# Performance work log

Hardware: AMD Instinct MI355X
Metric: run time of the kernel (lower is better)

Reference implementation:

```python
import jax, jax.numpy as jnp
import numpy as np

CACHE_LEN = 1024
EPS = 1e-5

def layer_norm(x, g, b):
    m = jnp.mean(x, axis=-1, keepdims=True)
    var = jnp.mean(jnp.square(x - m), axis=-1, keepdims=True)
    return (x - m) * jax.lax.rsqrt(var + EPS) * g + b

def setup_inputs() -> dict:
    key = jax.random.key(0)
    ks = jax.random.split(key, 16)
    B, Lq, Lk, D_IN, D_OUT = 4, 4096, 5119, 512, 512
    s = 1.0 / np.sqrt(D_IN)
    return {
        "q": jax.random.normal(ks[0], (B, Lq, D_IN), jnp.float32),
        "k": jax.random.normal(ks[1], (B, Lk, D_IN), jnp.float32),
        "v": jax.random.normal(ks[2], (B, Lk, D_IN), jnp.float32),
        "gq": jnp.ones((D_IN,), jnp.float32),
        "bq": jnp.zeros((D_IN,), jnp.float32),
        "gk": jnp.ones((D_IN,), jnp.float32),
        "bk": jnp.zeros((D_IN,), jnp.float32),
        "gv": jnp.ones((D_IN,), jnp.float32),
        "bv": jnp.zeros((D_IN,), jnp.float32),
        "Wq": jax.random.uniform(ks[3], (D_IN, D_OUT), jnp.float32, -s, s),
        "bwq": jax.random.uniform(ks[4], (D_OUT,), jnp.float32, -s, s),
        "Wk": jax.random.uniform(ks[5], (D_IN, D_OUT), jnp.float32, -s, s),
        "bwk": jax.random.uniform(ks[6], (D_OUT,), jnp.float32, -s, s),
        "Wv": jax.random.uniform(ks[7], (D_IN, D_OUT), jnp.float32, -s, s),
        "bwv": jax.random.uniform(ks[8], (D_OUT,), jnp.float32, -s, s),
    }

def reference(q, k, v, gq, bq, gk, bk, gv, bv, Wq, bwq, Wk, bwk, Wv, bwv):
    B, Lq, _ = q.shape
    Lk = k.shape[1]
    qp = layer_norm(q, gq, bq) @ Wq + bwq            # [B,Lq,Do]
    kp = layer_norm(k, gk, bk) @ Wk + bwk            # [B,Lk,Do]
    vp = layer_norm(v, gv, bv) @ Wv + bwv            # [B,Lk,Do]
    kv = jax.nn.relu(kp) * vp                         # [B,Lk,Do]
    # integrate3 skew-pad builds a banded ones mask: query row i attends to
    # kv columns [sup+i, sup+i+cache_len-1]. Equivalent sliding-window sum
    # computed via prefix sums (O(Lk*d) instead of O(Lq*Lk*d)).
    sup = Lk - Lq - CACHE_LEN + 1
    cs = jnp.cumsum(kv, axis=1)
    cs = jnp.concatenate([jnp.zeros_like(cs[:, :1]), cs], axis=1)  # [B,Lk+1,Do]
    starts = sup + jnp.arange(Lq)
    weighted = cs[:, starts + CACHE_LEN] - cs[:, starts]            # [B,Lq,Do]
    return jax.nn.relu(qp) * weighted
```

## Files before the change

### kernel.cpp

```cpp
#include <hip/hip_runtime.h>

#define B     4
#define LQ    4096
#define LK    5119
#define LKP   5120
#define D     512
#define CACHE 1024
#define MQ    (B * LQ)
#define MKP   (B * LKP)
#define NCH   160
#define TI    32

typedef float  f32x4  __attribute__((ext_vector_type(4)));
typedef __bf16 bf16x2 __attribute__((ext_vector_type(2)));
typedef __bf16 bf16x4 __attribute__((ext_vector_type(4)));
typedef __bf16 bf16x8 __attribute__((ext_vector_type(8)));

__device__ __forceinline__ void async16(void* lds, const void* g)
{
    __builtin_amdgcn_global_load_lds(
        (__attribute__((address_space(1))) void*)(g),
        (__attribute__((address_space(3))) void*)(lds),
        16, 0, 0);
}

__global__ __launch_bounds__(256) void prep_kernel(
    const float* __restrict__ q, const float* __restrict__ k,
    const float* __restrict__ v,
    const float* __restrict__ gq, const float* __restrict__ bq,
    const float* __restrict__ gk, const float* __restrict__ bk,
    const float* __restrict__ gv, const float* __restrict__ bv,
    const float* __restrict__ Wq, const float* __restrict__ Wk,
    const float* __restrict__ Wv,
    __bf16* __restrict__ qn, __bf16* __restrict__ kn, __bf16* __restrict__ vn,
    __bf16* __restrict__ wtq, __bf16* __restrict__ wtk, __bf16* __restrict__ wtv)
{
    const int z = blockIdx.y;

    if (z == 3) {
        const int idx = blockIdx.x;
        if (idx >= 384) return;
        const int zz  = idx >> 7;
        const int rem = idx & 127;
        const float* W = (zz == 0) ? Wq : (zz == 1) ? Wk : Wv;
        __bf16*     Wt = (zz == 0) ? wtq : (zz == 1) ? wtk : wtv;
        const int n  = (rem & 1) * 256 + threadIdx.x;
        const int k0 = (rem >> 1) * 8;
        bf16x8 o;
#pragma unroll
        for (int j = 0; j < 8; ++j)
            o[j] = (__bf16)W[(long)(k0 + j) * D + n];
        *reinterpret_cast<bf16x8*>(Wt + (long)n * D + k0) = o;
        return;
    }

    const float *x, *g, *bb; __bf16* o;
    if (z == 0)      { x = q; g = gq; bb = bq; o = qn; }
    else if (z == 1) { x = k; g = gk; bb = bk; o = kn; }
    else             { x = v; g = gv; bb = bv; o = vn; }

    const int nrows = (z == 0) ? MQ : MKP;
    const int wid   = threadIdx.x >> 6;
    const int lane  = threadIdx.x & 63;
    const int rp    = blockIdx.x * 4 + wid;
    if (rp >= nrows) return;

    long rin; bool valid = true;
    if (z == 0) rin = rp;
    else {
        const int bch = rp / LKP;
        int i = rp - bch * LKP;
        if (i == LK) { valid = false; i = LK - 1; }
        rin = (long)bch * LK + i;
    }

    const int    c0 = lane * 4;
    const float* xr = x + rin * D;

    const float4 a0 = *reinterpret_cast<const float4*>(xr + c0);
    const float4 a1 = *reinterpret_cast<const float4*>(xr + 256 + c0);

    float s  = a0.x + a0.y + a0.z + a0.w + a1.x + a1.y + a1.z + a1.w;
    float ss = a0.x*a0.x + a0.y*a0.y + a0.z*a0.z + a0.w*a0.w
             + a1.x*a1.x + a1.y*a1.y + a1.z*a1.z + a1.w*a1.w;
#pragma unroll
    for (int m = 1; m <= 32; m <<= 1) {
        s  += __shfl_xor(s,  m, 64);
        ss += __shfl_xor(ss, m, 64);
    }
    const float mean = s * (1.f / (float)D);
    const float var  = ss * (1.f / (float)D) - mean * mean;
    const float rs   = rsqrtf(var + 1e-5f);

    const float4 g0 = *reinterpret_cast<const float4*>(g  + c0);
    const float4 g1 = *reinterpret_cast<const float4*>(g  + 256 + c0);
    const float4 b0 = *reinterpret_cast<const float4*>(bb + c0);
    const float4 b1 = *reinterpret_cast<const float4*>(bb + 256 + c0);

    bf16x4 o0, o1;
    o0[0] = (__bf16)((a0.x - mean) * rs * g0.x + b0.x);
    o0[1] = (__bf16)((a0.y - mean) * rs * g0.y + b0.y);
    o0[2] = (__bf16)((a0.z - mean) * rs * g0.z + b0.z);
    o0[3] = (__bf16)((a0.w - mean) * rs * g0.w + b0.w);
    o1[0] = (__bf16)((a1.x - mean) * rs * g1.x + b1.x);
    o1[1] = (__bf16)((a1.y - mean) * rs * g1.y + b1.y);
    o1[2] = (__bf16)((a1.z - mean) * rs * g1.z + b1.z);
    o1[3] = (__bf16)((a1.w - mean) * rs * g1.w + b1.w);

    if (valid) {
        __bf16* orow = o + (long)rp * D;
        *reinterpret_cast<bf16x4*>(orow + c0)       = o0;
        *reinterpret_cast<bf16x4*>(orow + 256 + c0) = o1;
    }
}

__global__ __launch_bounds__(256, 2) void gemm_fused_kernel(
    const __bf16* __restrict__ qn, const __bf16* __restrict__ kn,
    const __bf16* __restrict__ vn,
    const __bf16* __restrict__ wtq, const __bf16* __restrict__ wtk,
    const __bf16* __restrict__ wtv,
    const float* __restrict__ bwq, const float* __restrict__ bwk,
    const float* __restrict__ bwv,
    __bf16* __restrict__ qpb, __bf16* __restrict__ kvb,
    float* __restrict__ Csum)
{
    __shared__ __attribute__((aligned(16))) __bf16 smem[32768];

    const int bid  = blockIdx.x;
    const int tid  = threadIdx.x;
    const int lane = tid & 63;
    const int wave = tid >> 6;
    const int quad = lane >> 4;
    const int l16  = lane & 15;
    const int wm   = wave >> 1;
    const int wn   = wave & 1;
    const int lrow = lane >> 3;
    const int lcs  = ((lane & 7) ^ lrow) * 8;

    if (bid < 640) {
        __bf16* Ks  = smem;
        __bf16* Vs  = smem + 8192;
        __bf16* WKs = smem + 16384;
        __bf16* WVs = smem + 24576;

        const int ntile = bid / 160;
        const int mtile = bid - ntile * 160;

        f32x4 acck[4][4], accv[4][4];
#pragma unroll
        for (int i = 0; i < 4; ++i)
#pragma unroll
            for (int j = 0; j < 4; ++j) {
                acck[i][j] = (f32x4){0.f, 0.f, 0.f, 0.f};
                accv[i][j] = (f32x4){0.f, 0.f, 0.f, 0.f};
            }

        const long arow0 = (long)mtile * 128;
        const long brow0 = (long)ntile * 128;

        auto stage_kv = [&](int kk) {
#pragma unroll
            for (int j = 0; j < 4; ++j) {
                const int r0  = (j * 4 + wave) * 8;
                const int row = r0 + lrow;
                async16(&Ks [r0 * 64], &kn [(arow0 + row) * D + kk + lcs]);
                async16(&Vs [r0 * 64], &vn [(arow0 + row) * D + kk + lcs]);
                async16(&WKs[r0 * 64], &wtk[(brow0 + row) * D + kk + lcs]);
                async16(&WVs[r0 * 64], &wtv[(brow0 + row) * D + kk + lcs]);
            }
        };

        stage_kv(0);
        for (int kt = 0; kt < 8; ++kt) {
            __syncthreads();

            bf16x8 fa[4][2], fb[4][2];
#pragma unroll
            for (int tm = 0; tm < 4; ++tm) {
                const int m = wm * 64 + tm * 16 + l16;
#pragma unroll
                for (int kh = 0; kh < 2; ++kh)
                    fa[tm][kh] = *reinterpret_cast<const bf16x8*>(
                        &Ks[m * 64 + (((kh * 4 + quad) ^ (m & 7)) * 8)]);
            }
#pragma unroll
            for (int tn = 0; tn < 4; ++tn) {
                const int n = wn * 64 + tn * 16 + l16;
#pragma unroll
                for (int kh = 0; kh < 2; ++kh)
                    fb[tn][kh] = *reinterpret_cast<const bf16x8*>(
                        &WKs[n * 64 + (((kh * 4 + quad) ^ (n & 7)) * 8)]);
            }
#pragma unroll
            for (int kh = 0; kh < 2; ++kh)
#pragma unroll
                for (int tm = 0; tm < 4; ++tm)
#pragma unroll
                    for (int tn = 0; tn < 4; ++tn)
                        acck[tm][tn] = __builtin_amdgcn_mfma_f32_16x16x32_bf16(
                            fa[tm][kh], fb[tn][kh], acck[tm][tn], 0, 0, 0);
#pragma unroll
            for (int tm = 0; tm < 4; ++tm) {
                const int m = wm * 64 + tm * 16 + l16;
#pragma unroll
                for (int kh = 0; kh < 2; ++kh)
                    fa[tm][kh] = *reinterpret_cast<const bf16x8*>(
                        &Vs[m * 64 + (((kh * 4 + quad) ^ (m & 7)) * 8)]);
            }
#pragma unroll
            for (int tn = 0; tn < 4; ++tn) {
                const int n = wn * 64 + tn * 16 + l16;
#pragma unroll
                for (int kh = 0; kh < 2; ++kh)
                    fb[tn][kh] = *reinterpret_cast<const bf16x8*>(
                        &WVs[n * 64 + (((kh * 4 + quad) ^ (n & 7)) * 8)]);
            }
            __syncthreads();
            if (kt < 7) stage_kv((kt + 1) * 64);
#pragma unroll
            for (int kh = 0; kh < 2; ++kh)
#pragma unroll
                for (int tm = 0; tm < 4; ++tm)
#pragma unroll
                    for (int tn = 0; tn < 4; ++tn)
                        accv[tm][tn] = __builtin_amdgcn_mfma_f32_16x16x32_bf16(
                            fa[tm][kh], fb[tn][kh], accv[tm][tn], 0, 0, 0);
        }

        float part[4][2];
#pragma unroll
        for (int tn = 0; tn < 4; ++tn) { part[tn][0] = 0.f; part[tn][1] = 0.f; }
#pragma unroll
        for (int tm = 0; tm < 4; ++tm) {
            const long row0 = arow0 + wm * 64 + tm * 16 + quad * 4;
#pragma unroll
            for (int tn = 0; tn < 4; ++tn) {
                const int col = (int)brow0 + wn * 64 + tn * 16 + l16;
                const float bkc = bwk[col];
                const float bvc = bwv[col];
#pragma unroll
                for (int r = 0; r < 4; ++r) {
                    const float kp = fmaxf(acck[tm][tn][r] + bkc, 0.f);
                    const float vp = accv[tm][tn][r] + bvc;
                    const __bf16 kb = (__bf16)(kp * vp);
                    kvb[(row0 + r) * D + col] = kb;
                    part[tn][tm >> 1] += (float)kb;
                }
            }
        }
#pragma unroll
        for (int tn = 0; tn < 4; ++tn)
#pragma unroll
            for (int th = 0; th < 2; ++th) {
                float vv = part[tn][th];
                vv += __shfl_xor(vv, 16, 64);
                vv += __shfl_xor(vv, 32, 64);
                if (quad == 0) {
                    const int fc = ((int)(arow0 >> 5)) + wm * 2 + th;
                    const int bb = fc / NCH;
                    const int cc = fc - bb * NCH;
                    const int col = (int)brow0 + wn * 64 + tn * 16 + l16;
                    Csum[((long)bb * NCH + cc) * D + col] = vv;
                }
            }
    } else {
        __bf16* Asb[2] = { smem,         smem + 16384 };
        __bf16* Bsb[2] = { smem + 8192,  smem + 24576 };

        const int bidq = bid - 640;

        f32x4 acc[4][4];
#pragma unroll
        for (int i = 0; i < 4; ++i)
#pragma unroll
            for (int j = 0; j < 4; ++j)
                acc[i][j] = (f32x4){0.f, 0.f, 0.f, 0.f};

        const long arow0 = (long)(bidq & 127) * 128;
        const long brow0 = (long)(bidq >> 7) * 128;

        auto stage_q = [&](int kk, int p) {
#pragma unroll
            for (int j = 0; j < 4; ++j) {
                const int r0  = (j * 4 + wave) * 8;
                const int row = r0 + lrow;
                async16(&Asb[p][r0 * 64], &qn [(arow0 + row) * D + kk + lcs]);
                async16(&Bsb[p][r0 * 64], &wtq[(brow0 + row) * D + kk + lcs]);
            }
        };

        stage_q(0, 0);
        __syncthreads();
        for (int kt = 0; kt < 8; ++kt) {
            const int p = kt & 1;
            if (kt < 7) stage_q((kt + 1) * 64, p ^ 1);

            bf16x8 af[4][2], bf[4][2];
#pragma unroll
            for (int tm = 0; tm < 4; ++tm) {
                const int m = wm * 64 + tm * 16 + l16;
#pragma unroll
                for (int kh = 0; kh < 2; ++kh)
                    af[tm][kh] = *reinterpret_cast<const bf16x8*>(
                        &Asb[p][m * 64 + (((kh * 4 + quad) ^ (m & 7)) * 8)]);
            }
#pragma unroll
            for (int tn = 0; tn < 4; ++tn) {
                const int n = wn * 64 + tn * 16 + l16;
#pragma unroll
                for (int kh = 0; kh < 2; ++kh)
                    bf[tn][kh] = *reinterpret_cast<const bf16x8*>(
                        &Bsb[p][n * 64 + (((kh * 4 + quad) ^ (n & 7)) * 8)]);
            }
#pragma unroll
            for (int kh = 0; kh < 2; ++kh)
#pragma unroll
                for (int tm = 0; tm < 4; ++tm)
#pragma unroll
                    for (int tn = 0; tn < 4; ++tn)
                        acc[tm][tn] = __builtin_amdgcn_mfma_f32_16x16x32_bf16(
                            af[tm][kh], bf[tn][kh], acc[tm][tn], 0, 0, 0);
            if (kt < 7) __syncthreads();
        }

#pragma unroll
        for (int tm = 0; tm < 4; ++tm) {
            const long row0 = arow0 + wm * 64 + tm * 16 + quad * 4;
#pragma unroll
            for (int tn = 0; tn < 4; ++tn) {
                const int col = (int)brow0 + wn * 64 + tn * 16 + l16;
                const float bv = bwq[col];
#pragma unroll
                for (int r = 0; r < 4; ++r)
                    qpb[(row0 + r) * D + col] =
                        (__bf16)fmaxf(acc[tm][tn][r] + bv, 0.f);
            }
        }
    }
}

__global__ __launch_bounds__(256) void window_kernel(
    const __bf16* __restrict__ kv, const float* __restrict__ Csum,
    const __bf16* __restrict__ qpb, float* __restrict__ out)
{
    const int iq   = blockIdx.x;
    const int b    = blockIdx.y;
    const int i0   = iq * TI;
    const int col2 = threadIdx.x * 2;

    const float* cs = Csum + (long)b * NCH * D + col2;
    float s0 = 0.f, s1 = 0.f;
#pragma unroll
    for (int c = 0; c < 32; ++c) {
        const float2 cv = *reinterpret_cast<const float2*>(cs + (long)(iq + c) * D);
        s0 += cv.x; s1 += cv.y;
    }

    const __bf16* kvb = kv  + (long)b * LKP * D + col2;
    const __bf16* qb  = qpb + (long)b * LQ  * D + col2;
    float*        ob  = out + (long)b * LQ  * D + col2;

#pragma unroll 8
    for (int i = i0; i < i0 + TI; ++i) {
        const bf16x2 qv = *reinterpret_cast<const bf16x2*>(qb + (long)i * D);
        *reinterpret_cast<float2*>(ob + (long)i * D) =
            make_float2((float)qv[0] * s0, (float)qv[1] * s1);
        const bf16x2 lead  = *reinterpret_cast<const bf16x2*>(kvb + (long)(i + CACHE) * D);
        const bf16x2 trail = *reinterpret_cast<const bf16x2*>(kvb + (long)i * D);
        s0 += (float)lead[0] - (float)trail[0];
        s1 += (float)lead[1] - (float)trail[1];
    }
}

extern "C" void kernel_launch(void* const* d_in, const int* in_sizes, int n_in,
                              void* d_out, int out_size, void* d_ws, size_t ws_size,
                              hipStream_t stream)
{
    const float* q   = (const float*)d_in[0];
    const float* k   = (const float*)d_in[1];
    const float* v   = (const float*)d_in[2];
    const float* gq  = (const float*)d_in[3];
    const float* bq  = (const float*)d_in[4];
    const float* gk  = (const float*)d_in[5];
    const float* bk  = (const float*)d_in[6];
    const float* gv  = (const float*)d_in[7];
    const float* bv  = (const float*)d_in[8];
    const float* Wq  = (const float*)d_in[9];
    const float* bwq = (const float*)d_in[10];
    const float* Wk  = (const float*)d_in[11];
    const float* bwk = (const float*)d_in[12];
    const float* Wv  = (const float*)d_in[13];
    const float* bwv = (const float*)d_in[14];
    float* out = (float*)d_out;

    char* ws = (char*)d_ws;
    __bf16* qn   = (__bf16*)ws;
    __bf16* kn   = qn  + (long)MQ  * D;
    __bf16* vn   = kn  + (long)MKP * D;
    __bf16* qpb  = vn  + (long)MKP * D;
    __bf16* kvb  = qpb + (long)MQ  * D;
    __bf16* wtq  = kvb + (long)MKP * D;
    __bf16* wtk  = wtq + (long)D * D;
    __bf16* wtv  = wtk + (long)D * D;
    float*  Csum = (float*)(wtv + (long)D * D);

    prep_kernel<<<dim3(5120, 4), 256, 0, stream>>>(
        q, k, v, gq, bq, gk, bk, gv, bv, Wq, Wk, Wv,
        qn, kn, vn, wtq, wtk, wtv);

    gemm_fused_kernel<<<640 + 512, 256, 0, stream>>>(
        qn, kn, vn, wtq, wtk, wtv, bwq, bwk, bwv, qpb, kvb, Csum);

    window_kernel<<<dim3(LQ / TI, B), 256, 0, stream>>>(kvb, Csum, qpb, out);
}
```

Baseline: 227.7 us.

## Split fused K/V projection into two sequential double-buffered GEMMs

The K and V projection blocks previously ran both GEMMs interleaved, holding two accumulator sets and single-buffered shared tiles. They now run two back-to-back passes of a shared double-buffered 128x128 GEMM routine, which the Q path also uses. This is meant to overlap global-to-LDS loads with MFMA work and cut live fragment registers. In exchange, the pipeline drains and refills between the K and V passes, and the kv blocks perform two full K-loops.

```diff
diff --git a/kernel.cpp b/kernel.cpp
--- a/kernel.cpp
+++ b/kernel.cpp
@@ -137,59 +137,44 @@
     const int lrow = lane >> 3;
     const int lcs  = ((lane & 7) ^ lrow) * 8;
 
-    if (bid < 640) {
-        __bf16* Ks  = smem;
-        __bf16* Vs  = smem + 8192;
-        __bf16* WKs = smem + 16384;
-        __bf16* WVs = smem + 24576;
-
-        const int ntile = bid / 160;
-        const int mtile = bid - ntile * 160;
-
-        f32x4 acck[4][4], accv[4][4];
-#pragma unroll
-        for (int i = 0; i < 4; ++i)
-#pragma unroll
-            for (int j = 0; j < 4; ++j) {
-                acck[i][j] = (f32x4){0.f, 0.f, 0.f, 0.f};
-                accv[i][j] = (f32x4){0.f, 0.f, 0.f, 0.f};
-            }
-
-        const long arow0 = (long)mtile * 128;
-        const long brow0 = (long)ntile * 128;
-
-        auto stage_kv = [&](int kk) {
+    auto gemm128 = [&](const __bf16* __restrict__ A,
+                       const __bf16* __restrict__ Bt,
+                       f32x4 (&acc)[4][4], long arow0, long brow0) {
+        auto stg = [&](int kk, int p) {
+            __bf16* As = smem + p * 16384;
+            __bf16* Bs = smem + 8192 + p * 16384;
 #pragma unroll
             for (int j = 0; j < 4; ++j) {
                 const int r0  = (j * 4 + wave) * 8;
                 const int row = r0 + lrow;
-                async16(&Ks [r0 * 64], &kn [(arow0 + row) * D + kk + lcs]);
-                async16(&Vs [r0 * 64], &vn [(arow0 + row) * D + kk + lcs]);
-                async16(&WKs[r0 * 64], &wtk[(brow0 + row) * D + kk + lcs]);
-                async16(&WVs[r0 * 64], &wtv[(brow0 + row) * D + kk + lcs]);
+                async16(&As[r0 * 64], &A [(arow0 + row) * D + kk + lcs]);
+                async16(&Bs[r0 * 64], &Bt[(brow0 + row) * D + kk + lcs]);
             }
         };
-
-        stage_kv(0);
+        stg(0, 0);
+        __syncthreads();
         for (int kt = 0; kt < 8; ++kt) {
-            __syncthreads();
-
-            bf16x8 fa[4][2], fb[4][2];
+            const int p = kt & 1;
+            if (kt < 7) stg((kt + 1) * 64, p ^ 1);
+
+            const __bf16* As = smem + p * 16384;
+            const __bf16* Bs = smem + 8192 + p * 16384;
+            bf16x8 af[4][2], bf[4][2];
 #pragma unroll
             for (int tm = 0; tm < 4; ++tm) {
                 const int m = wm * 64 + tm * 16 + l16;
 #pragma unroll
                 for (int kh = 0; kh < 2; ++kh)
-                    fa[tm][kh] = *reinterpret_cast<const bf16x8*>(
-                        &Ks[m * 64 + (((kh * 4 + quad) ^ (m & 7)) * 8)]);
+                    af[tm][kh] = *reinterpret_cast<const bf16x8*>(
+                        &As[m * 64 + (((kh * 4 + quad) ^ (m & 7)) * 8)]);
             }
 #pragma unroll
             for (int tn = 0; tn < 4; ++tn) {
                 const int n = wn * 64 + tn * 16 + l16;
 #pragma unroll
                 for (int kh = 0; kh < 2; ++kh)
-                    fb[tn][kh] = *reinterpret_cast<const bf16x8*>(
-                        &WKs[n * 64 + (((kh * 4 + quad) ^ (n & 7)) * 8)]);
+                    bf[tn][kh] = *reinterpret_cast<const bf16x8*>(
+                        &Bs[n * 64 + (((kh * 4 + quad) ^ (n & 7)) * 8)]);
             }
 #pragma unroll
             for (int kh = 0; kh < 2; ++kh)
@@ -197,35 +182,33 @@
                 for (int tm = 0; tm < 4; ++tm)
 #pragma unroll
                     for (int tn = 0; tn < 4; ++tn)
-                        acck[tm][tn] = __builtin_amdgcn_mfma_f32_16x16x32_bf16(
-                            fa[tm][kh], fb[tn][kh], acck[tm][tn], 0, 0, 0);
-#pragma unroll
-            for (int tm = 0; tm < 4; ++tm) {
-                const int m = wm * 64 + tm * 16 + l16;
-#pragma unroll
-                for (int kh = 0; kh < 2; ++kh)
-                    fa[tm][kh] = *reinterpret_cast<const bf16x8*>(
-                        &Vs[m * 64 + (((kh * 4 + quad) ^ (m & 7)) * 8)]);
-            }
-#pragma unroll
-            for (int tn = 0; tn < 4; ++tn) {
-                const int n = wn * 64 + tn * 16 + l16;
-#pragma unroll
-                for (int kh = 0; kh < 2; ++kh)
-                    fb[tn][kh] = *reinterpret_cast<const bf16x8*>(
-                        &WVs[n * 64 + (((kh * 4 + quad) ^ (n & 7)) * 8)]);
-            }
-            __syncthreads();
-            if (kt < 7) stage_kv((kt + 1) * 64);
-#pragma unroll
-            for (int kh = 0; kh < 2; ++kh)
-#pragma unroll
-                for (int tm = 0; tm < 4; ++tm)
-#pragma unroll
-                    for (int tn = 0; tn < 4; ++tn)
-                        accv[tm][tn] = __builtin_amdgcn_mfma_f32_16x16x32_bf16(
-                            fa[tm][kh], fb[tn][kh], accv[tm][tn], 0, 0, 0);
+                        acc[tm][tn] = __builtin_amdgcn_mfma_f32_16x16x32_bf16(
+                            af[tm][kh], bf[tn][kh], acc[tm][tn], 0, 0, 0);
+            if (kt < 7) __syncthreads();
         }
+    };
+
+    if (bid < 640) {
+        const int ntile = bid / 160;
+        const int mtile = bid - ntile * 160;
+        const long arow0 = (long)mtile * 128;
+        const long brow0 = (long)ntile * 128;
+
+        f32x4 acck[4][4];
+#pragma unroll
+        for (int i = 0; i < 4; ++i)
+#pragma unroll
+            for (int j = 0; j < 4; ++j)
+                acck[i][j] = (f32x4){0.f, 0.f, 0.f, 0.f};
+        gemm128(kn, wtk, acck, arow0, brow0);
+
+        f32x4 accv[4][4];
+#pragma unroll
+        for (int i = 0; i < 4; ++i)
+#pragma unroll
+            for (int j = 0; j < 4; ++j)
+                accv[i][j] = (f32x4){0.f, 0.f, 0.f, 0.f};
+        gemm128(vn, wtv, accv, arow0, brow0);
 
         float part[4][2];
 #pragma unroll
@@ -264,10 +247,9 @@
                 }
             }
     } else {
-        __bf16* Asb[2] = { smem,         smem + 16384 };
-        __bf16* Bsb[2] = { smem + 8192,  smem + 24576 };
-
         const int bidq = bid - 640;
+        const long arow0 = (long)(bidq & 127) * 128;
+        const long brow0 = (long)(bidq >> 7) * 128;
 
         f32x4 acc[4][4];
 #pragma unroll
@@ -275,53 +257,7 @@
 #pragma unroll
             for (int j = 0; j < 4; ++j)
                 acc[i][j] = (f32x4){0.f, 0.f, 0.f, 0.f};
-
-        const long arow0 = (long)(bidq & 127) * 128;
-        const long brow0 = (long)(bidq >> 7) * 128;
-
-        auto stage_q = [&](int kk, int p) {
-#pragma unroll
-            for (int j = 0; j < 4; ++j) {
-                const int r0  = (j * 4 + wave) * 8;
-                const int row = r0 + lrow;
-                async16(&Asb[p][r0 * 64], &qn [(arow0 + row) * D + kk + lcs]);
-                async16(&Bsb[p][r0 * 64], &wtq[(brow0 + row) * D + kk + lcs]);
-            }
-        };
-
-        stage_q(0, 0);
-        __syncthreads();
-        for (int kt = 0; kt < 8; ++kt) {
-            const int p = kt & 1;
-            if (kt < 7) stage_q((kt + 1) * 64, p ^ 1);
-
-            bf16x8 af[4][2], bf[4][2];
-#pragma unroll
-            for (int tm = 0; tm < 4; ++tm) {
-                const int m = wm * 64 + tm * 16 + l16;
-#pragma unroll
-                for (int kh = 0; kh < 2; ++kh)
-                    af[tm][kh] = *reinterpret_cast<const bf16x8*>(
-                        &Asb[p][m * 64 + (((kh * 4 + quad) ^ (m & 7)) * 8)]);
-            }
-#pragma unroll
-            for (int tn = 0; tn < 4; ++tn) {
-                const int n = wn * 64 + tn * 16 + l16;
-#pragma unroll
-                for (int kh = 0; kh < 2; ++kh)
-                    bf[tn][kh] = *reinterpret_cast<const bf16x8*>(
-                        &Bsb[p][n * 64 + (((kh * 4 + quad) ^ (n & 7)) * 8)]);
-            }
-#pragma unroll
-            for (int kh = 0; kh < 2; ++kh)
-#pragma unroll
-                for (int tm = 0; tm < 4; ++tm)
-#pragma unroll
-                    for (int tn = 0; tn < 4; ++tn)
-                        acc[tm][tn] = __builtin_amdgcn_mfma_f32_16x16x32_bf16(
-                            af[tm][kh], bf[tn][kh], acc[tm][tn], 0, 0, 0);
-            if (kt < 7) __syncthreads();
-        }
+        gemm128(qn, wtq, acc, arow0, brow0);
 
 #pragma unroll
         for (int tm = 0; tm < 4; ++tm) {
```

Result: no change. 225.9 us (-0.8%).
